# Kernel tuning notes

Hardware: AMD Instinct MI355X
Metric: run time of the kernel (lower is better)

## Reference

```python
import jax, jax.numpy as jnp
import numpy as np

TOKENS = 16384
INPUT_DIM = 2048
NUM_EXPERTS = 16
K = 2


def setup_inputs() -> dict:
    key = jax.random.key(0)
    kx, kn, kw, kb = jax.random.split(key, 4)
    x = jax.random.normal(kx, (TOKENS, INPUT_DIM), dtype=jnp.float32)
    noise = jax.random.normal(kn, (TOKENS, NUM_EXPERTS), dtype=jnp.float32)
    # nn.Linear params: weight [out, in], bias [out]; kaiming-uniform-ish init
    bound = 1.0 / np.sqrt(INPUT_DIM)
    W = jax.random.uniform(kw, (NUM_EXPERTS, INPUT_DIM), dtype=jnp.float32, minval=-bound, maxval=bound)
    b = jax.random.uniform(kb, (NUM_EXPERTS,), dtype=jnp.float32, minval=-bound, maxval=bound)
    return {"x": x, "noise": noise, "W": W, "b": b}


def reference(x, noise, W, b):
    # logits: [tokens, num_experts]
    logits = jnp.einsum("td,ed->te", x, W) + b
    noisy_logits = logits + noise * 0.1
    top_k_values, top_k_indices = jax.lax.top_k(noisy_logits, K)  # [tokens, K]
    weights = jax.nn.softmax(top_k_values, axis=-1)               # [tokens, K]
    # scatter weights back into dense [tokens, num_experts] (zeros elsewhere)
    one_hot = jax.nn.one_hot(top_k_indices, NUM_EXPERTS, dtype=logits.dtype)  # [tokens, K, E]
    sparse_weights = jnp.einsum("tke,tk->te", one_hot, weights)
    return sparse_weights
```

## Files before the change

### kernel.cpp

```cpp
#include <hip/hip_runtime.h>
#include <hip/hip_bf16.h>
#include <math.h>

#define TOKENS 16384
#define DIM    2048
#define NEXP   16

typedef float fvec4 __attribute__((ext_vector_type(4)));


__device__ __forceinline__ float fma4(fvec4 a, fvec4 w, float acc) {
    return fmaf(a.x, w.x, fmaf(a.y, w.y, fmaf(a.z, w.z, fmaf(a.w, w.w, acc))));
}

__global__ __launch_bounds__(256, 2) void gating_moe_kernel(
    const float* __restrict__ x,
    const float* __restrict__ noise,
    const float* __restrict__ W,
    const float* __restrict__ b,
    float* __restrict__ out)
{
    const int tid   = threadIdx.x;
    const int lane  = tid & 63;
    const int waveI = tid >> 6;
    const int sub   = lane & 31;
    const int tgroup = lane >> 5;
    const int wave_base = blockIdx.x * 32 + waveI * 8;
    const int t0 = wave_base + tgroup * 4;

    float acc[4][NEXP];
#pragma unroll
    for (int t = 0; t < 4; ++t)
#pragma unroll
        for (int e = 0; e < NEXP; ++e) acc[t][e] = 0.0f;

    const fvec4* __restrict__ xr = (const fvec4*)(x + (size_t)t0 * DIM);
    const fvec4* __restrict__ Wv = (const fvec4*)W;
    const int ROW = DIM / 4;

#pragma unroll 2
    for (int j = 0; j < 16; ++j) {
        const int idx = j * 32 + sub;
        fvec4 xv[4];
#pragma unroll
        for (int t = 0; t < 4; ++t) xv[t] = xr[t * ROW + idx];

        fvec4 wv[8];
#pragma unroll
        for (int e = 0; e < 8; ++e) wv[e] = Wv[e * ROW + idx];
#pragma unroll
        for (int e = 0; e < 8; ++e)
#pragma unroll
            for (int t = 0; t < 4; ++t)
                acc[t][e] = fma4(xv[t], wv[e], acc[t][e]);

#pragma unroll
        for (int e = 0; e < 8; ++e) wv[e] = Wv[(e + 8) * ROW + idx];
#pragma unroll
        for (int e = 0; e < 8; ++e)
#pragma unroll
            for (int t = 0; t < 4; ++t)
                acc[t][e + 8] = fma4(xv[t], wv[e], acc[t][e + 8]);
    }

#pragma unroll
    for (int t = 0; t < 4; ++t)
#pragma unroll
        for (int e = 0; e < NEXP; ++e) {
            float v = acc[t][e];
            v += __shfl_xor(v, 1);
            v += __shfl_xor(v, 2);
            v += __shfl_xor(v, 4);
            v += __shfl_xor(v, 8);
            v += __shfl_xor(v, 16);
            acc[t][e] = v;
        }

    const int tsel  = (lane >> 3) & 3;
    const int token = wave_base + (lane >> 3);

    float full[NEXP];
#pragma unroll
    for (int e = 0; e < NEXP; ++e) {
        float v = acc[0][e];
        v = (tsel == 1) ? acc[1][e] : v;
        v = (tsel == 2) ? acc[2][e] : v;
        v = (tsel == 3) ? acc[3][e] : v;
        full[e] = v;
    }

    const fvec4* __restrict__ nz4 = (const fvec4*)(noise + (size_t)token * NEXP);
    float noisy[NEXP];
#pragma unroll
    for (int q = 0; q < 4; ++q) {
        fvec4 nv = nz4[q];
        noisy[q * 4 + 0] = full[q * 4 + 0] + b[q * 4 + 0] + 0.1f * nv.x;
        noisy[q * 4 + 1] = full[q * 4 + 1] + b[q * 4 + 1] + 0.1f * nv.y;
        noisy[q * 4 + 2] = full[q * 4 + 2] + b[q * 4 + 2] + 0.1f * nv.z;
        noisy[q * 4 + 3] = full[q * 4 + 3] + b[q * 4 + 3] + 0.1f * nv.w;
    }

    float v1 = -INFINITY; int i1 = -1;
#pragma unroll
    for (int e = 0; e < NEXP; ++e) {
        bool g = noisy[e] > v1;
        v1 = g ? noisy[e] : v1;
        i1 = g ? e : i1;
    }
    float v2 = -INFINITY; int i2 = -1;
#pragma unroll
    for (int e = 0; e < NEXP; ++e) {
        bool g = (e != i1) && (noisy[e] > v2);
        v2 = g ? noisy[e] : v2;
        i2 = g ? e : i2;
    }

    float d  = __expf(v2 - v1);
    float w1 = 1.0f / (1.0f + d);
    float w2 = d * w1;

    const int e0 = (lane & 7) * 2;
    const int e1 = e0 + 1;
    float o0 = (e0 == i1) ? w1 : ((e0 == i2) ? w2 : 0.0f);
    float o1 = (e1 == i1) ? w1 : ((e1 == i2) ? w2 : 0.0f);
    float2 o = make_float2(o0, o1);
    ((float2*)(out + (size_t)token * NEXP))[lane & 7] = o;
}

extern "C" void kernel_launch(void* const* d_in, const int* in_sizes, int n_in,
                              void* d_out, int out_size, void* d_ws, size_t ws_size,
                              hipStream_t stream) {
    const float* x     = (const float*)d_in[0];
    const float* noise = (const float*)d_in[1];
    const float* W     = (const float*)d_in[2];
    const float* b     = (const float*)d_in[3];
    float* out = (float*)d_out;

    dim3 grid(TOKENS / 32);
    dim3 block(256);
    gating_moe_kernel<<<grid, block, 0, stream>>>(x, noise, W, b, out);
}
```

Baseline: 211.3 us.

## Stage router weights in LDS and halve tokens per wave with 512-thread blocks

Each block now cooperatively loads the 16x2048 router weight matrix into shared memory in two halves and reads W from LDS instead of global/L1. Each wave handles 4 tokens (2 per half-wave) instead of 8, with 512 threads per block, cutting accumulator registers so more waves can stay resident. The cost is two extra block-wide barriers and a full reload of W into LDS per block. Global x traffic stays the same, and the kernel is memory-bound on x, so any gain depends on better latency hiding.

```diff
diff --git a/kernel.cpp b/kernel.cpp
--- a/kernel.cpp
+++ b/kernel.cpp
@@ -13,58 +13,69 @@
     return fmaf(a.x, w.x, fmaf(a.y, w.y, fmaf(a.z, w.z, fmaf(a.w, w.w, acc))));
 }
 
-__global__ __launch_bounds__(256, 2) void gating_moe_kernel(
+__global__ __launch_bounds__(512, 4) void gating_moe_kernel(
     const float* __restrict__ x,
     const float* __restrict__ noise,
     const float* __restrict__ W,
     const float* __restrict__ b,
     float* __restrict__ out)
 {
-    const int tid   = threadIdx.x;
-    const int lane  = tid & 63;
-    const int waveI = tid >> 6;
-    const int sub   = lane & 31;
+    __shared__ fvec4 Wl[NEXP * 256];
+
+    const int tid    = threadIdx.x;
+    const int lane   = tid & 63;
+    const int waveI  = tid >> 6;
+    const int sub    = lane & 31;
     const int tgroup = lane >> 5;
-    const int wave_base = blockIdx.x * 32 + waveI * 8;
-    const int t0 = wave_base + tgroup * 4;
+    const int wave_base = blockIdx.x * 32 + waveI * 4;
+    const int t0 = wave_base + tgroup * 2;
 
-    float acc[4][NEXP];
+    float acc[2][NEXP];
 #pragma unroll
-    for (int t = 0; t < 4; ++t)
+    for (int t = 0; t < 2; ++t)
 #pragma unroll
         for (int e = 0; e < NEXP; ++e) acc[t][e] = 0.0f;
 
     const fvec4* __restrict__ xr = (const fvec4*)(x + (size_t)t0 * DIM);
-    const fvec4* __restrict__ Wv = (const fvec4*)W;
-    const int ROW = DIM / 4;
-
-#pragma unroll 2
-    for (int j = 0; j < 16; ++j) {
-        const int idx = j * 32 + sub;
-        fvec4 xv[4];
-#pragma unroll
-        for (int t = 0; t < 4; ++t) xv[t] = xr[t * ROW + idx];
-
-        fvec4 wv[8];
-#pragma unroll
-        for (int e = 0; e < 8; ++e) wv[e] = Wv[e * ROW + idx];
-#pragma unroll
-        for (int e = 0; e < 8; ++e)
-#pragma unroll
-            for (int t = 0; t < 4; ++t)
-                acc[t][e] = fma4(xv[t], wv[e], acc[t][e]);
+    const fvec4* __restrict__ Wg = (const fvec4*)W;
 
 #pragma unroll
-        for (int e = 0; e < 8; ++e) wv[e] = Wv[(e + 8) * ROW + idx];
+    for (int h = 0; h < 2; ++h) {
+        if (h) __syncthreads();
 #pragma unroll
-        for (int e = 0; e < 8; ++e)
+        for (int t = 0; t < 8; ++t) {
+            const int i = tid + t * 512;
+            const int e = i >> 8, c = i & 255;
+            Wl[i] = Wg[e * 512 + h * 256 + c];
+        }
+        __syncthreads();
+
 #pragma unroll
-            for (int t = 0; t < 4; ++t)
-                acc[t][e + 8] = fma4(xv[t], wv[e], acc[t][e + 8]);
+        for (int jj = 0; jj < 8; ++jj) {
+            const int idx = jj * 32 + sub;
+            fvec4 xv0 = xr[0 * 512 + h * 256 + idx];
+            fvec4 xv1 = xr[1 * 512 + h * 256 + idx];
+
+            fvec4 wv[8];
+#pragma unroll
+            for (int e = 0; e < 8; ++e) wv[e] = Wl[e * 256 + idx];
+#pragma unroll
+            for (int e = 0; e < 8; ++e) {
+                acc[0][e] = fma4(xv0, wv[e], acc[0][e]);
+                acc[1][e] = fma4(xv1, wv[e], acc[1][e]);
+            }
+#pragma unroll
+            for (int e = 0; e < 8; ++e) wv[e] = Wl[(e + 8) * 256 + idx];
+#pragma unroll
+            for (int e = 0; e < 8; ++e) {
+                acc[0][e + 8] = fma4(xv0, wv[e], acc[0][e + 8]);
+                acc[1][e + 8] = fma4(xv1, wv[e], acc[1][e + 8]);
+            }
+        }
     }
 
 #pragma unroll
-    for (int t = 0; t < 4; ++t)
+    for (int t = 0; t < 2; ++t)
 #pragma unroll
         for (int e = 0; e < NEXP; ++e) {
             float v = acc[t][e];
@@ -76,18 +87,13 @@
             acc[t][e] = v;
         }
 
-    const int tsel  = (lane >> 3) & 3;
-    const int token = wave_base + (lane >> 3);
+    const int tsel  = (lane >> 4) & 1;
+    const int token = wave_base + (lane >> 4);
 
     float full[NEXP];
 #pragma unroll
-    for (int e = 0; e < NEXP; ++e) {
-        float v = acc[0][e];
-        v = (tsel == 1) ? acc[1][e] : v;
-        v = (tsel == 2) ? acc[2][e] : v;
-        v = (tsel == 3) ? acc[3][e] : v;
-        full[e] = v;
-    }
+    for (int e = 0; e < NEXP; ++e)
+        full[e] = tsel ? acc[1][e] : acc[0][e];
 
     const fvec4* __restrict__ nz4 = (const fvec4*)(noise + (size_t)token * NEXP);
     float noisy[NEXP];
@@ -119,12 +125,9 @@
     float w1 = 1.0f / (1.0f + d);
     float w2 = d * w1;
 
-    const int e0 = (lane & 7) * 2;
-    const int e1 = e0 + 1;
-    float o0 = (e0 == i1) ? w1 : ((e0 == i2) ? w2 : 0.0f);
-    float o1 = (e1 == i1) ? w1 : ((e1 == i2) ? w2 : 0.0f);
-    float2 o = make_float2(o0, o1);
-    ((float2*)(out + (size_t)token * NEXP))[lane & 7] = o;
+    const int e = lane & 15;
+    float o = (e == i1) ? w1 : ((e == i2) ? w2 : 0.0f);
+    out[(size_t)wave_base * NEXP + lane] = o;
 }
 
 extern "C" void kernel_launch(void* const* d_in, const int* in_sizes, int n_in,
@@ -137,6 +140,6 @@
     float* out = (float*)d_out;
 
     dim3 grid(TOKENS / 32);
-    dim3 block(256);
+    dim3 block(512);
     gating_moe_kernel<<<grid, block, 0, stream>>>(x, noise, W, b, out);
 }
```

Result: slower. 238.8 us (+13.1%).
